# Performance work log

Hardware: AMD Instinct MI355X
Metric: run time of the kernel (lower is better)

The kernel has to match this reference:

```python
import jax, jax.numpy as jnp
import numpy as np

HEADS = 8
DIM_HEAD = 64
DIM = 512
EPS = 1e-5


def setup_inputs() -> dict:
    key = jax.random.key(0)
    ks = jax.random.split(key, 4)
    b, n = 4, 2048
    inner = HEADS * DIM_HEAD
    x = jax.random.normal(ks[0], (b, n, DIM), dtype=jnp.float32)
    pose_bias = jax.random.normal(ks[1], (b, n), dtype=jnp.float32)
    ln_gamma = jnp.ones((DIM,), dtype=jnp.float32)
    ln_beta = jnp.zeros((DIM,), dtype=jnp.float32)
    w_qkv = jax.random.normal(ks[2], (DIM, 3 * inner), dtype=jnp.float32) * (DIM ** -0.5)
    w_out = jax.random.normal(ks[3], (inner, DIM), dtype=jnp.float32) * (inner ** -0.5)
    beta = jnp.float32(0.5)
    return {"x": x, "pose_bias": pose_bias, "ln_gamma": ln_gamma,
            "ln_beta": ln_beta, "w_qkv": w_qkv, "w_out": w_out, "beta": beta}


def reference(x, pose_bias, ln_gamma, ln_beta, w_qkv, w_out, beta):
    b, n, d = x.shape
    h, dh = HEADS, DIM_HEAD
    scale = dh ** -0.5
    # LayerNorm (biased variance, eps=1e-5, affine)
    mu = jnp.mean(x, axis=-1, keepdims=True)
    var = jnp.mean(jnp.square(x - mu), axis=-1, keepdims=True)
    xn = (x - mu) * jax.lax.rsqrt(var + EPS) * ln_gamma + ln_beta
    # fused QKV projection (no bias)
    qkv = xn @ w_qkv                                  # [b, n, 3*h*dh]
    q, k, v = jnp.split(qkv, 3, axis=-1)
    def to_heads(t):
        return t.reshape(b, n, h, dh).transpose(0, 2, 1, 3)  # [b, h, n, dh]
    q, k, v = to_heads(q), to_heads(k), to_heads(v)
    dots = jnp.einsum('bhnd,bhmd->bhnm', q, k) * scale  # [b, h, n, n]
    # additive pose bias: beta * (bias_i + bias_j), broadcast over heads
    pose_attn = beta * (pose_bias[:, None, :, None] + pose_bias[:, None, None, :])
    dots = dots + pose_attn
    attn = jax.nn.softmax(dots, axis=-1)
    out = jnp.einsum('bhnm,bhmd->bhnd', attn, v)       # [b, h, n, dh]
    out = out.transpose(0, 2, 1, 3).reshape(b, n, h * dh)
    return out @ w_out
```

## Files before the change

### kernel.cpp

```cpp
#include <hip/hip_runtime.h>

#define NH    8
#define DH    64
#define DIMD  512
#define NCTX  2048
#define NB    4
#define NROWS (NB * NCTX)
#define QKVN  (3 * DIMD)

typedef __attribute__((ext_vector_type(8))) short bf16x8;
typedef __attribute__((ext_vector_type(4))) float f32x4;

#define INV_LN2 1.44269504f
#define SCLOG   (0.125f * INV_LN2)

__device__ __forceinline__ unsigned short f2bits(float f) {
  unsigned u = __float_as_uint(f);
  u += 0x7fffu + ((u >> 16) & 1u);
  return (unsigned short)(u >> 16);
}
__device__ __forceinline__ float bits2f(unsigned short u) {
  return __uint_as_float(((unsigned)u) << 16);
}

__global__ __launch_bounds__(256) void ln_kernel(
    const float* __restrict__ x,
    const float* __restrict__ gamma,
    const float* __restrict__ beta,
    unsigned short* __restrict__ xn) {
  const int wid  = threadIdx.x >> 6;
  const int lane = threadIdx.x & 63;
  const int row  = blockIdx.x * 4 + wid;
  const float* xr = x + (size_t)row * DIMD + lane * 8;
  float v[8];
  const float4 a = *reinterpret_cast<const float4*>(xr);
  const float4 b = *reinterpret_cast<const float4*>(xr + 4);
  v[0] = a.x; v[1] = a.y; v[2] = a.z; v[3] = a.w;
  v[4] = b.x; v[5] = b.y; v[6] = b.z; v[7] = b.w;
  float s = 0.f;
#pragma unroll
  for (int i = 0; i < 8; ++i) s += v[i];
#pragma unroll
  for (int off = 32; off; off >>= 1) s += __shfl_down(s, off);
  s = __shfl(s, 0);
  const float mu = s * (1.f / DIMD);
  float ss = 0.f;
#pragma unroll
  for (int i = 0; i < 8; ++i) { float d = v[i] - mu; ss += d * d; }
#pragma unroll
  for (int off = 32; off; off >>= 1) ss += __shfl_down(ss, off);
  ss = __shfl(ss, 0);
  const float inv = rsqrtf(ss * (1.f / DIMD) + 1e-5f);
  const float4 g0 = *reinterpret_cast<const float4*>(gamma + lane * 8);
  const float4 g1 = *reinterpret_cast<const float4*>(gamma + lane * 8 + 4);
  const float4 b0 = *reinterpret_cast<const float4*>(beta + lane * 8);
  const float4 b1 = *reinterpret_cast<const float4*>(beta + lane * 8 + 4);
  float g[8] = {g0.x, g0.y, g0.z, g0.w, g1.x, g1.y, g1.z, g1.w};
  float be[8] = {b0.x, b0.y, b0.z, b0.w, b1.x, b1.y, b1.z, b1.w};
  bf16x8 o;
#pragma unroll
  for (int i = 0; i < 8; ++i)
    o[i] = (short)f2bits((v[i] - mu) * inv * g[i] + be[i]);
  *reinterpret_cast<bf16x8*>(xn + (size_t)row * DIMD + lane * 8) = o;
}

__global__ __launch_bounds__(256) void tconv_kernel(
    const float* __restrict__ in0, unsigned short* __restrict__ out0,
    const float* __restrict__ in1, unsigned short* __restrict__ out1) {
  const int z = blockIdx.z;
  const int C = z ? DIMD : QKVN;
  if (z && blockIdx.x >= DIMD / 64) return;
  const float* in = z ? in1 : in0;
  unsigned short* out = z ? out1 : out0;
  __shared__ float T[64][65];
  const int r0 = blockIdx.y * 64, c0 = blockIdx.x * 64;
  const int ty = threadIdx.x >> 4, tx = threadIdx.x & 15;
#pragma unroll
  for (int i = 0; i < 4; ++i) {
    const int r = ty + i * 16;
    const float4 v = *reinterpret_cast<const float4*>(
        in + (size_t)(r0 + r) * C + c0 + tx * 4);
    T[r][tx * 4 + 0] = v.x; T[r][tx * 4 + 1] = v.y;
    T[r][tx * 4 + 2] = v.z; T[r][tx * 4 + 3] = v.w;
  }
  __syncthreads();
#pragma unroll
  for (int i = 0; i < 4; ++i) {
    const int c = ty + i * 16;
    ushort4 o;
    o.x = f2bits(T[tx * 4 + 0][c]); o.y = f2bits(T[tx * 4 + 1][c]);
    o.z = f2bits(T[tx * 4 + 2][c]); o.w = f2bits(T[tx * 4 + 3][c]);
    *reinterpret_cast<ushort4*>(out + (size_t)(c0 + c) * DIMD + r0 + tx * 4) = o;
  }
}

__global__ __launch_bounds__(256) void vtrans_kernel(
    const unsigned short* __restrict__ qkv,
    const float* __restrict__ pb,
    const float* __restrict__ betap,
    unsigned short* __restrict__ cexp,
    unsigned short* __restrict__ vt) {
  __shared__ unsigned short T[64][68];
  const int jt = blockIdx.x, hi = blockIdx.y, bi = blockIdx.z;
  const int ty = threadIdx.x >> 4, tx = threadIdx.x & 15;
  const int j0 = jt * 64;
#pragma unroll
  for (int i = 0; i < 4; ++i) {
    const int j = ty + i * 16;
    const ushort4 v = *reinterpret_cast<const ushort4*>(
        qkv + (size_t)(bi * NCTX + j0 + j) * QKVN + 2 * DIMD + hi * DH + tx * 4);
    T[j][tx * 4 + 0] = v.x; T[j][tx * 4 + 1] = v.y;
    T[j][tx * 4 + 2] = v.z; T[j][tx * 4 + 3] = v.w;
  }
  const float bl2 = betap[0] * INV_LN2;
  const float4 pv = *reinterpret_cast<const float4*>(pb + bi * NCTX + j0 + tx * 4);
  ushort4 cb;
  cb.x = f2bits(exp2f(bl2 * pv.x)); cb.y = f2bits(exp2f(bl2 * pv.y));
  cb.z = f2bits(exp2f(bl2 * pv.z)); cb.w = f2bits(exp2f(bl2 * pv.w));
  if (hi == 0 && ty == 0)
    *reinterpret_cast<ushort4*>(cexp + bi * NCTX + j0 + tx * 4) = cb;
  const float c0 = bits2f(cb.x), c1 = bits2f(cb.y), c2 = bits2f(cb.z), c3 = bits2f(cb.w);
  __syncthreads();
#pragma unroll
  for (int i = 0; i < 4; ++i) {
    const int d = ty + i * 16;
    ushort4 o;
    o.x = f2bits(bits2f(T[tx * 4 + 0][d]) * c0);
    o.y = f2bits(bits2f(T[tx * 4 + 1][d]) * c1);
    o.z = f2bits(bits2f(T[tx * 4 + 2][d]) * c2);
    o.w = f2bits(bits2f(T[tx * 4 + 3][d]) * c3);
    *reinterpret_cast<ushort4*>(
        vt + ((size_t)(bi * NH + hi) * DH + d) * NCTX + j0 + tx * 4) = o;
  }
}

__device__ __forceinline__ void storeC(float* C, size_t idx, float v) { C[idx] = v; }
__device__ __forceinline__ void storeC(unsigned short* C, size_t idx, float v) { C[idx] = f2bits(v); }

template <typename CT, bool QS>
__global__ __launch_bounds__(256) void mgemm_kernel(
    const unsigned short* __restrict__ A, const unsigned short* __restrict__ Bt,
    CT* __restrict__ C, int M, int N, int K) {
  __shared__ __align__(16) unsigned short As[128][72];
  __shared__ __align__(16) unsigned short Bs[128][72];
  const int tid  = threadIdx.x;
  const int wave = tid >> 6, lane = tid & 63;
  const int quad = lane >> 4, l16 = lane & 15;
  const int wr = wave >> 1, wc = wave & 1;
  const int tm0 = blockIdx.y * 128, tn0 = blockIdx.x * 128;
  const int srow = tid >> 3;
  const int schunk = (tid & 7) * 8;
  f32x4 acc[4][4];
#pragma unroll
  for (int i = 0; i < 4; ++i)
#pragma unroll
    for (int j = 0; j < 4; ++j) acc[i][j] = (f32x4){0.f, 0.f, 0.f, 0.f};

  bf16x8 ra[4], rb[4];
#pragma unroll
  for (int p = 0; p < 4; ++p) {
    const int r = srow + p * 32;
    ra[p] = *reinterpret_cast<const bf16x8*>(A + (size_t)(tm0 + r) * K + schunk);
    rb[p] = *reinterpret_cast<const bf16x8*>(Bt + (size_t)(tn0 + r) * K + schunk);
  }
  for (int k0 = 0; k0 < K; k0 += 64) {
#pragma unroll
    for (int p = 0; p < 4; ++p) {
      const int r = srow + p * 32;
      *reinterpret_cast<bf16x8*>(&As[r][schunk]) = ra[p];
      *reinterpret_cast<bf16x8*>(&Bs[r][schunk]) = rb[p];
    }
    __syncthreads();
    if (k0 + 64 < K) {
#pragma unroll
      for (int p = 0; p < 4; ++p) {
        const int r = srow + p * 32;
        ra[p] = *reinterpret_cast<const bf16x8*>(A + (size_t)(tm0 + r) * K + k0 + 64 + schunk);
        rb[p] = *reinterpret_cast<const bf16x8*>(Bt + (size_t)(tn0 + r) * K + k0 + 64 + schunk);
      }
    }
#pragma unroll
    for (int kc = 0; kc < 2; ++kc) {
      const int kk = kc * 32 + quad * 8;
      bf16x8 af[4], bfr[4];
#pragma unroll
      for (int i = 0; i < 4; ++i)
        af[i] = *reinterpret_cast<const bf16x8*>(&As[wr * 64 + i * 16 + l16][kk]);
#pragma unroll
      for (int j = 0; j < 4; ++j)
        bfr[j] = *reinterpret_cast<const bf16x8*>(&Bs[wc * 64 + j * 16 + l16][kk]);
#pragma unroll
      for (int i = 0; i < 4; ++i)
#pragma unroll
        for (int j = 0; j < 4; ++j)
          acc[i][j] = __builtin_amdgcn_mfma_f32_16x16x32_bf16(af[i], bfr[j], acc[i][j], 0, 0, 0);
    }
    __syncthreads();
  }
#pragma unroll
  for (int j = 0; j < 4; ++j) {
    const int col = tn0 + wc * 64 + j * 16 + l16;
    const float scl = (QS && col < DIMD) ? SCLOG : 1.0f;
#pragma unroll
    for (int i = 0; i < 4; ++i)
#pragma unroll
      for (int r = 0; r < 4; ++r)
        storeC(C, (size_t)(tm0 + wr * 64 + i * 16 + quad * 4 + r) * N + col,
               acc[i][j][r] * scl);
  }
}

__global__ __launch_bounds__(256, 4) void fattn_kernel(
    const unsigned short* __restrict__ qkv,
    const unsigned short* __restrict__ vtg,
    const unsigned short* __restrict__ cexp,
    unsigned short* __restrict__ out) {
  __shared__ __align__(16) unsigned short lds[9280];
  unsigned short (*Kl)[72] = (unsigned short (*)[72])(lds);
  unsigned short (*Vt)[72] = (unsigned short (*)[72])(lds + 4608);
  unsigned short* crow = lds + 9216;
  unsigned short* Ob = lds;
  float* lb = (float*)(lds + 4352);

  const int qt = blockIdx.x, hi = blockIdx.y, bi = blockIdx.z;
  const int tid  = threadIdx.x;
  const int wave = tid >> 6, lane = tid & 63;
  const int quad = lane >> 4, l16 = lane & 15;
  const int wq = wave & 1, wk = wave >> 1;
  const int qrow0 = qt * 64;
  const unsigned short* base  = qkv + (size_t)bi * NCTX * QKVN + hi * DH;
  const unsigned short* vbase = vtg + (size_t)(bi * NH + hi) * DH * NCTX;
  const unsigned short* cbase = cexp + (size_t)bi * NCTX;
  const int sr = tid >> 2;
  const int sc4 = (tid & 3) * 16;

  bf16x8 qf[2][2];
#pragma unroll
  for (int u = 0; u < 2; ++u)
#pragma unroll
    for (int h = 0; h < 2; ++h)
      qf[u][h] = *reinterpret_cast<const bf16x8*>(
          base + (size_t)(qrow0 + wq * 32 + u * 16 + l16) * QKVN + h * 32 + quad * 8);
  bf16x8 pk0, pk1, pv0, pv1; ushort4 pc;
  {
    const unsigned short* kr = base + (size_t)sr * QKVN + DIMD + sc4;
    pk0 = *reinterpret_cast<const bf16x8*>(kr);
    pk1 = *reinterpret_cast<const bf16x8*>(kr + 8);
    const unsigned short* vr = vbase + (size_t)sr * NCTX + sc4;
    pv0 = *reinterpret_cast<const bf16x8*>(vr);
    pv1 = *reinterpret_cast<const bf16x8*>(vr + 8);
    if (tid < 16) pc = *reinterpret_cast<const ushort4*>(cbase + tid * 4);
    *reinterpret_cast<bf16x8*>(&Kl[sr][sc4])     = pk0;
    *reinterpret_cast<bf16x8*>(&Kl[sr][sc4 + 8]) = pk1;
    *reinterpret_cast<bf16x8*>(&Vt[sr][sc4])     = pv0;
    *reinterpret_cast<bf16x8*>(&Vt[sr][sc4 + 8]) = pv1;
    if (tid < 16) *reinterpret_cast<ushort4*>(&crow[tid * 4]) = pc;
  }
  __syncthreads();

  f32x4 O[2][4], accl[2];
#pragma unroll
  for (int u = 0; u < 2; ++u) {
    accl[u] = (f32x4){0.f, 0.f, 0.f, 0.f};
#pragma unroll
    for (int s = 0; s < 4; ++s) O[u][s] = (f32x4){0.f, 0.f, 0.f, 0.f};
  }

  for (int kt = 0; kt < 32; ++kt) {
    if (kt < 31) {
      const int krow1 = (kt + 1) * 64;
      const unsigned short* kr = base + (size_t)(krow1 + sr) * QKVN + DIMD + sc4;
      pk0 = *reinterpret_cast<const bf16x8*>(kr);
      pk1 = *reinterpret_cast<const bf16x8*>(kr + 8);
      const unsigned short* vr = vbase + (size_t)sr * NCTX + krow1 + sc4;
      pv0 = *reinterpret_cast<const bf16x8*>(vr);
      pv1 = *reinterpret_cast<const bf16x8*>(vr + 8);
      if (tid < 16) pc = *reinterpret_cast<const ushort4*>(cbase + krow1 + tid * 4);
    }
    f32x4 sfr[2][2];
#pragma unroll
    for (int t = 0; t < 2; ++t) {
      const bf16x8 kf0 = *reinterpret_cast<const bf16x8*>(
          &Kl[wk * 32 + t * 16 + l16][quad * 8]);
      const bf16x8 kf1 = *reinterpret_cast<const bf16x8*>(
          &Kl[wk * 32 + t * 16 + l16][32 + quad * 8]);
#pragma unroll
      for (int u = 0; u < 2; ++u) {
        f32x4 acc = (f32x4){0.f, 0.f, 0.f, 0.f};
        acc = __builtin_amdgcn_mfma_f32_16x16x32_bf16(kf0, qf[u][0], acc, 0, 0, 0);
        acc = __builtin_amdgcn_mfma_f32_16x16x32_bf16(kf1, qf[u][1], acc, 0, 0, 0);
        sfr[t][u] = acc;
      }
    }
    bf16x8 pf[2];
#pragma unroll
    for (int u = 0; u < 2; ++u) {
      unsigned x0, x1, y0, y1;
      {
        const float e0 = exp2f(sfr[0][u][0]), e1 = exp2f(sfr[0][u][1]);
        const float e2 = exp2f(sfr[0][u][2]), e3 = exp2f(sfr[0][u][3]);
        const float f0 = exp2f(sfr[1][u][0]), f1 = exp2f(sfr[1][u][1]);
        const float f2 = exp2f(sfr[1][u][2]), f3 = exp2f(sfr[1][u][3]);
        asm("v_cvt_pk_bf16_f32 %0, %1, %2" : "=v"(x0) : "v"(e0), "v"(e1));
        asm("v_cvt_pk_bf16_f32 %0, %1, %2" : "=v"(x1) : "v"(e2), "v"(e3));
        asm("v_cvt_pk_bf16_f32 %0, %1, %2" : "=v"(y0) : "v"(f0), "v"(f1));
        asm("v_cvt_pk_bf16_f32 %0, %1, %2" : "=v"(y1) : "v"(f2), "v"(f3));
      }
      asm("v_permlane32_swap_b32 %0, %1" : "+v"(x0), "+v"(y0));
      asm("v_permlane32_swap_b32 %0, %1" : "+v"(x1), "+v"(y1));
      asm("v_permlane16_swap_b32 %0, %1" : "+v"(x0), "+v"(y0));
      asm("v_permlane16_swap_b32 %0, %1" : "+v"(x1), "+v"(y1));
      union { unsigned q[4]; bf16x8 v; } pu;
      pu.q[0] = x0; pu.q[1] = x1; pu.q[2] = y0; pu.q[3] = y1;
      pf[u] = pu.v;
    }
    {
      const bf16x8 cf = *reinterpret_cast<const bf16x8*>(&crow[wk * 32 + quad * 8]);
      accl[0] = __builtin_amdgcn_mfma_f32_16x16x32_bf16(pf[0], cf, accl[0], 0, 0, 0);
      accl[1] = __builtin_amdgcn_mfma_f32_16x16x32_bf16(pf[1], cf, accl[1], 0, 0, 0);
#pragma unroll
      for (int s = 0; s < 4; ++s) {
        const bf16x8 bv = *reinterpret_cast<const bf16x8*>(
            &Vt[s * 16 + l16][wk * 32 + quad * 8]);
        O[0][s] = __builtin_amdgcn_mfma_f32_16x16x32_bf16(pf[0], bv, O[0][s], 0, 0, 0);
        O[1][s] = __builtin_amdgcn_mfma_f32_16x16x32_bf16(pf[1], bv, O[1][s], 0, 0, 0);
      }
    }
    if (kt < 31) {
      __syncthreads();
      *reinterpret_cast<bf16x8*>(&Kl[sr][sc4])     = pk0;
      *reinterpret_cast<bf16x8*>(&Kl[sr][sc4 + 8]) = pk1;
      *reinterpret_cast<bf16x8*>(&Vt[sr][sc4])     = pv0;
      *reinterpret_cast<bf16x8*>(&Vt[sr][sc4 + 8]) = pv1;
      if (tid < 16) *reinterpret_cast<ushort4*>(&crow[tid * 4]) = pc;
      __syncthreads();
    }
  }
  __syncthreads();
  if (wk == 1) {
#pragma unroll
    for (int u = 0; u < 2; ++u) {
#pragma unroll
      for (int s = 0; s < 4; ++s)
#pragma unroll
        for (int r = 0; r < 4; ++r)
          Ob[(wq * 32 + u * 16 + quad * 4 + r) * 68 + s * 16 + l16] = f2bits(O[u][s][r]);
      if (l16 == 0)
#pragma unroll
        for (int r = 0; r < 4; ++r)
          lb[64 + wq * 32 + u * 16 + quad * 4 + r] = accl[u][r];
    }
  } else {
#pragma unroll
    for (int u = 0; u < 2; ++u)
      if (l16 == 0)
#pragma unroll
        for (int r = 0; r < 4; ++r)
          lb[wq * 32 + u * 16 + quad * 4 + r] = accl[u][r];
  }
  __syncthreads();
  if (wk == 0) {
#pragma unroll
    for (int u = 0; u < 2; ++u)
#pragma unroll
      for (int r = 0; r < 4; ++r) {
        const int ql = wq * 32 + u * 16 + quad * 4 + r;
        const float linv = 1.f / (lb[ql] + lb[64 + ql]);
        const size_t orow = ((size_t)bi * NCTX + qrow0 + ql) * DIMD + hi * DH;
#pragma unroll
        for (int s = 0; s < 4; ++s)
          out[orow + s * 16 + l16] =
              f2bits((O[u][s][r] + bits2f(Ob[ql * 68 + s * 16 + l16])) * linv);
      }
  }
}

extern "C" void kernel_launch(void* const* d_in, const int* in_sizes, int n_in,
                              void* d_out, int out_size, void* d_ws, size_t ws_size,
                              hipStream_t stream) {
  const float* x     = (const float*)d_in[0];
  const float* pose  = (const float*)d_in[1];
  const float* gam   = (const float*)d_in[2];
  const float* bet   = (const float*)d_in[3];
  const float* wqkv  = (const float*)d_in[4];
  const float* wout  = (const float*)d_in[5];
  const float* betap = (const float*)d_in[6];
  float* out = (float*)d_out;

  unsigned short* xn    = (unsigned short*)d_ws;
  unsigned short* qkvb  = xn + (size_t)NROWS * DIMD;
  unsigned short* wqkvT = qkvb + (size_t)NROWS * QKVN;
  unsigned short* woutT = wqkvT + (size_t)QKVN * DIMD;
  unsigned short* vtg   = woutT + (size_t)DIMD * DIMD;
  unsigned short* cexp  = vtg + (size_t)NB * NH * DH * NCTX;
  unsigned short* aout  = xn;

  ln_kernel<<<NROWS / 4, 256, 0, stream>>>(x, gam, bet, xn);
  tconv_kernel<<<dim3(QKVN / 64, DIMD / 64, 2), 256, 0, stream>>>(
      wqkv, wqkvT, wout, woutT);
  mgemm_kernel<unsigned short, true><<<dim3(QKVN / 128, NROWS / 128), 256, 0, stream>>>(
      xn, wqkvT, qkvb, NROWS, QKVN, DIMD);
  vtrans_kernel<<<dim3(NCTX / 64, NH, NB), 256, 0, stream>>>(
      qkvb, pose, betap, cexp, vtg);
  fattn_kernel<<<dim3(NCTX / 64, NH, NB), 256, 0, stream>>>(qkvb, vtg, cexp, aout);
  mgemm_kernel<float, false><<<dim3(DIMD / 128, NROWS / 128), 256, 0, stream>>>(
      aout, woutT, out, NROWS, DIMD, DIMD);
}
```

Baseline: 178.3 us.

## Use direct global-to-LDS loads with double buffering in attention and QKV GEMM

Adds a QKV GEMM variant and reworks the flash-attention kernel so that global_load_lds DMAs tiles straight into XOR-swizzled shared memory, skipping the round trip through registers. The attention kernel now double-buffers K, V and the exp-bias row in LDS, prefetching the next tile while computing on the current one, which removes one barrier per iteration. This aims to cut register pressure and load latency. In exchange it doubles attention LDS use, which may lower occupancy, and the new GEMM loads all of each K-step before a barrier without overlapping the next step.

```diff
diff --git a/kernel.cpp b/kernel.cpp
--- a/kernel.cpp
+++ b/kernel.cpp
@@ -21,6 +21,17 @@
 }
 __device__ __forceinline__ float bits2f(unsigned short u) {
   return __uint_as_float(((unsigned)u) << 16);
+}
+
+__device__ __forceinline__ void gll16(const void* g, void* l) {
+  __builtin_amdgcn_global_load_lds(
+      (const __attribute__((address_space(1))) unsigned int*)g,
+      (__attribute__((address_space(3))) unsigned int*)l, 16, 0, 0);
+}
+__device__ __forceinline__ void gll4(const void* g, void* l) {
+  __builtin_amdgcn_global_load_lds(
+      (const __attribute__((address_space(1))) unsigned int*)g,
+      (__attribute__((address_space(3))) unsigned int*)l, 4, 0, 0);
 }
 
 __global__ __launch_bounds__(256) void ln_kernel(
@@ -210,17 +221,72 @@
   }
 }
 
+template <typename CT, bool QS>
+__global__ __launch_bounds__(256) void ggemm_kernel(
+    const unsigned short* __restrict__ A, const unsigned short* __restrict__ Bt,
+    CT* __restrict__ C, int M, int N, int K) {
+  __shared__ __align__(16) unsigned short As[128 * 64];
+  __shared__ __align__(16) unsigned short Bs[128 * 64];
+  const int tid  = threadIdx.x;
+  const int wave = tid >> 6, lane = tid & 63;
+  const int quad = lane >> 4, l16 = lane & 15;
+  const int wr = wave >> 1, wc = wave & 1;
+  const int tm0 = blockIdx.y * 128, tn0 = blockIdx.x * 128;
+  const int srow = wave * 8 + (lane >> 3);
+  const int ssh  = (((lane & 7) * 16) ^ ((lane >> 3) << 4)) >> 1;
+  const unsigned short* ap = A + (size_t)(tm0 + srow) * K + ssh;
+  const unsigned short* bp = Bt + (size_t)(tn0 + srow) * K + ssh;
+  const int xs = (l16 & 7) << 3;
+  f32x4 acc[4][4];
+#pragma unroll
+  for (int i = 0; i < 4; ++i)
+#pragma unroll
+    for (int j = 0; j < 4; ++j) acc[i][j] = (f32x4){0.f, 0.f, 0.f, 0.f};
+
+  for (int k0 = 0; k0 < K; k0 += 64) {
+#pragma unroll
+    for (int i = 0; i < 4; ++i) {
+      gll16(ap + (size_t)(i * 32) * K + k0, &As[i * 2048 + wave * 512]);
+      gll16(bp + (size_t)(i * 32) * K + k0, &Bs[i * 2048 + wave * 512]);
+    }
+    __syncthreads();
+#pragma unroll
+    for (int kc = 0; kc < 2; ++kc) {
+      const int kk = ((kc * 32 + quad * 8) ^ xs);
+      bf16x8 af[4], bfr[4];
+#pragma unroll
+      for (int i = 0; i < 4; ++i)
+        af[i] = *reinterpret_cast<const bf16x8*>(&As[(wr * 64 + i * 16 + l16) * 64 + kk]);
+#pragma unroll
+      for (int j = 0; j < 4; ++j)
+        bfr[j] = *reinterpret_cast<const bf16x8*>(&Bs[(wc * 64 + j * 16 + l16) * 64 + kk]);
+#pragma unroll
+      for (int i = 0; i < 4; ++i)
+#pragma unroll
+        for (int j = 0; j < 4; ++j)
+          acc[i][j] = __builtin_amdgcn_mfma_f32_16x16x32_bf16(af[i], bfr[j], acc[i][j], 0, 0, 0);
+    }
+    __syncthreads();
+  }
+#pragma unroll
+  for (int j = 0; j < 4; ++j) {
+    const int col = tn0 + wc * 64 + j * 16 + l16;
+    const float scl = (QS && col < DIMD) ? SCLOG : 1.0f;
+#pragma unroll
+    for (int i = 0; i < 4; ++i)
+#pragma unroll
+      for (int r = 0; r < 4; ++r)
+        storeC(C, (size_t)(tm0 + wr * 64 + i * 16 + quad * 4 + r) * N + col,
+               acc[i][j][r] * scl);
+  }
+}
+
 __global__ __launch_bounds__(256, 4) void fattn_kernel(
     const unsigned short* __restrict__ qkv,
     const unsigned short* __restrict__ vtg,
     const unsigned short* __restrict__ cexp,
     unsigned short* __restrict__ out) {
-  __shared__ __align__(16) unsigned short lds[9280];
-  unsigned short (*Kl)[72] = (unsigned short (*)[72])(lds);
-  unsigned short (*Vt)[72] = (unsigned short (*)[72])(lds + 4608);
-  unsigned short* crow = lds + 9216;
-  unsigned short* Ob = lds;
-  float* lb = (float*)(lds + 4352);
+  __shared__ __align__(16) unsigned short lds[2][8320];
 
   const int qt = blockIdx.x, hi = blockIdx.y, bi = blockIdx.z;
   const int tid  = threadIdx.x;
@@ -231,8 +297,23 @@
   const unsigned short* base  = qkv + (size_t)bi * NCTX * QKVN + hi * DH;
   const unsigned short* vbase = vtg + (size_t)(bi * NH + hi) * DH * NCTX;
   const unsigned short* cbase = cexp + (size_t)bi * NCTX;
-  const int sr = tid >> 2;
-  const int sc4 = (tid & 3) * 16;
+
+  const int sr8 = lane >> 3;
+  const int ssh = ((((lane & 7) * 16) ^ (sr8 << 4)) >> 1);
+  const unsigned short* kp0 = base + (size_t)(wave * 8 + sr8) * QKVN + DIMD + ssh;
+  const unsigned short* kp1 = kp0 + (size_t)32 * QKVN;
+  const unsigned short* vp0 = vbase + (size_t)(wave * 8 + sr8) * NCTX + ssh;
+  const unsigned short* vp1 = vp0 + (size_t)32 * NCTX;
+  const unsigned short* cp  = cbase + (tid & 31) * 2;
+
+#define STAGE(buf)                                    \
+  gll16(kp0, &(buf)[wave * 512]);                     \
+  gll16(kp1, &(buf)[2048 + wave * 512]);              \
+  gll16(vp0, &(buf)[4096 + wave * 512]);              \
+  gll16(vp1, &(buf)[6144 + wave * 512]);              \
+  if (tid < 32) gll4(cp, &(buf)[8192]);               \
+  kp0 += (size_t)64 * QKVN; kp1 += (size_t)64 * QKVN; \
+  vp0 += 64; vp1 += 64; cp += 64;
 
   bf16x8 qf[2][2];
 #pragma unroll
@@ -241,21 +322,14 @@
     for (int h = 0; h < 2; ++h)
       qf[u][h] = *reinterpret_cast<const bf16x8*>(
           base + (size_t)(qrow0 + wq * 32 + u * 16 + l16) * QKVN + h * 32 + quad * 8);
-  bf16x8 pk0, pk1, pv0, pv1; ushort4 pc;
-  {
-    const unsigned short* kr = base + (size_t)sr * QKVN + DIMD + sc4;
-    pk0 = *reinterpret_cast<const bf16x8*>(kr);
-    pk1 = *reinterpret_cast<const bf16x8*>(kr + 8);
-    const unsigned short* vr = vbase + (size_t)sr * NCTX + sc4;
-    pv0 = *reinterpret_cast<const bf16x8*>(vr);
-    pv1 = *reinterpret_cast<const bf16x8*>(vr + 8);
-    if (tid < 16) pc = *reinterpret_cast<const ushort4*>(cbase + tid * 4);
-    *reinterpret_cast<bf16x8*>(&Kl[sr][sc4])     = pk0;
-    *reinterpret_cast<bf16x8*>(&Kl[sr][sc4 + 8]) = pk1;
-    *reinterpret_cast<bf16x8*>(&Vt[sr][sc4])     = pv0;
-    *reinterpret_cast<bf16x8*>(&Vt[sr][sc4 + 8]) = pv1;
-    if (tid < 16) *reinterpret_cast<ushort4*>(&crow[tid * 4]) = pc;
-  }
+
+  const int xs = (l16 & 7) << 3;
+  const int kofs0 = (wk * 32 + l16) * 64 + ((quad * 8) ^ xs);
+  const int kofs1 = (wk * 32 + l16) * 64 + ((32 + quad * 8) ^ xs);
+  const int vofs  = 4096 + l16 * 64 + ((wk * 32 + quad * 8) ^ xs);
+  const int cofs  = 8192 + wk * 32 + quad * 8;
+
+  STAGE(lds[0]);
   __syncthreads();
 
   f32x4 O[2][4], accl[2];
@@ -267,23 +341,13 @@
   }
 
   for (int kt = 0; kt < 32; ++kt) {
-    if (kt < 31) {
-      const int krow1 = (kt + 1) * 64;
-      const unsigned short* kr = base + (size_t)(krow1 + sr) * QKVN + DIMD + sc4;
-      pk0 = *reinterpret_cast<const bf16x8*>(kr);
-      pk1 = *reinterpret_cast<const bf16x8*>(kr + 8);
-      const unsigned short* vr = vbase + (size_t)sr * NCTX + krow1 + sc4;
-      pv0 = *reinterpret_cast<const bf16x8*>(vr);
-      pv1 = *reinterpret_cast<const bf16x8*>(vr + 8);
-      if (tid < 16) pc = *reinterpret_cast<const ushort4*>(cbase + krow1 + tid * 4);
-    }
+    const unsigned short* bc = lds[kt & 1];
+    if (kt < 31) { STAGE(lds[(kt & 1) ^ 1]); }
     f32x4 sfr[2][2];
 #pragma unroll
     for (int t = 0; t < 2; ++t) {
-      const bf16x8 kf0 = *reinterpret_cast<const bf16x8*>(
-          &Kl[wk * 32 + t * 16 + l16][quad * 8]);
-      const bf16x8 kf1 = *reinterpret_cast<const bf16x8*>(
-          &Kl[wk * 32 + t * 16 + l16][32 + quad * 8]);
+      const bf16x8 kf0 = *reinterpret_cast<const bf16x8*>(&bc[kofs0 + t * 1024]);
+      const bf16x8 kf1 = *reinterpret_cast<const bf16x8*>(&bc[kofs1 + t * 1024]);
 #pragma unroll
       for (int u = 0; u < 2; ++u) {
         f32x4 acc = (f32x4){0.f, 0.f, 0.f, 0.f};
@@ -315,28 +379,21 @@
       pf[u] = pu.v;
     }
     {
-      const bf16x8 cf = *reinterpret_cast<const bf16x8*>(&crow[wk * 32 + quad * 8]);
+      const bf16x8 cf = *reinterpret_cast<const bf16x8*>(&bc[cofs]);
       accl[0] = __builtin_amdgcn_mfma_f32_16x16x32_bf16(pf[0], cf, accl[0], 0, 0, 0);
       accl[1] = __builtin_amdgcn_mfma_f32_16x16x32_bf16(pf[1], cf, accl[1], 0, 0, 0);
 #pragma unroll
       for (int s = 0; s < 4; ++s) {
-        const bf16x8 bv = *reinterpret_cast<const bf16x8*>(
-            &Vt[s * 16 + l16][wk * 32 + quad * 8]);
+        const bf16x8 bv = *reinterpret_cast<const bf16x8*>(&bc[vofs + s * 1024]);
         O[0][s] = __builtin_amdgcn_mfma_f32_16x16x32_bf16(pf[0], bv, O[0][s], 0, 0, 0);
         O[1][s] = __builtin_amdgcn_mfma_f32_16x16x32_bf16(pf[1], bv, O[1][s], 0, 0, 0);
       }
     }
-    if (kt < 31) {
-      __syncthreads();
-      *reinterpret_cast<bf16x8*>(&Kl[sr][sc4])     = pk0;
-      *reinterpret_cast<bf16x8*>(&Kl[sr][sc4 + 8]) = pk1;
-      *reinterpret_cast<bf16x8*>(&Vt[sr][sc4])     = pv0;
-      *reinterpret_cast<bf16x8*>(&Vt[sr][sc4 + 8]) = pv1;
-      if (tid < 16) *reinterpret_cast<ushort4*>(&crow[tid * 4]) = pc;
-      __syncthreads();
-    }
-  }
-  __syncthreads();
+    __syncthreads();
+  }
+#undef STAGE
+  unsigned short* Ob = (unsigned short*)lds;
+  float* lb = (float*)((unsigned short*)lds + 4352);
   if (wk == 1) {
 #pragma unroll
     for (int u = 0; u < 2; ++u) {
@@ -398,7 +455,7 @@
   ln_kernel<<<NROWS / 4, 256, 0, stream>>>(x, gam, bet, xn);
   tconv_kernel<<<dim3(QKVN / 64, DIMD / 64, 2), 256, 0, stream>>>(
       wqkv, wqkvT, wout, woutT);
-  mgemm_kernel<unsigned short, true><<<dim3(QKVN / 128, NROWS / 128), 256, 0, stream>>>(
+  ggemm_kernel<unsigned short, true><<<dim3(QKVN / 128, NROWS / 128), 256, 0, stream>>>(
       xn, wqkvT, qkvb, NROWS, QKVN, DIMD);
   vtrans_kernel<<<dim3(NCTX / 64, NH, NB), 256, 0, stream>>>(
       qkvb, pose, betap, cexp, vtg);
```

After: 177.9 us. About the same (-0.2%).
